# Performance work log

Hardware: AMD Instinct MI355X
Metric: run time of the kernel (lower is better)

The kernel has to match this reference:

```python
import jax, jax.numpy as jnp
import numpy as np

DELTA_V = 0.5
DELTA_D = 1.5
ALPHA = 1.0
BETA = 1.0
GAMMA = 0.001
K = 33  # segment count: id 0 = background, 1..32 = instances (matches fill_max)


def setup_inputs() -> dict:
    key = jax.random.key(0)
    k1, k2 = jax.random.split(key)
    embeddings = jax.random.normal(k1, (8, 16, 512, 512), dtype=jnp.float32)
    instance_masks = jax.random.randint(k2, (8, 512, 512), 0, K, dtype=jnp.int32)
    return {"embeddings": embeddings, "instance_masks": instance_masks}


def _safe_norm(sq):
    # sqrt with zero-safe gradient: returns 0 where sq == 0
    pos = sq > 0
    return jnp.sqrt(jnp.where(pos, sq, 1.0)) * pos.astype(sq.dtype)


def _per_image(emb, mask):
    # emb: (E, H, W), mask: (H, W)
    E = emb.shape[0]
    emb_flat = emb.reshape(E, -1).T            # (N, E)
    ids = mask.reshape(-1)                      # (N,)

    counts = jax.ops.segment_sum(jnp.ones(ids.shape, jnp.float32), ids, num_segments=K)  # (K,)
    sums = jax.ops.segment_sum(emb_flat, ids, num_segments=K)                             # (K, E)
    counts_c = jnp.maximum(counts, 1.0)
    means = sums / counts_c[:, None]            # (K, E)

    present = counts[1:] > 0                    # (K-1,) which instance ids appear
    n_inst = present.sum().astype(jnp.float32)

    # variance (pull) term: per-pixel distance to own instance mean
    diff = emb_flat - means[ids]                # (N, E)
    pix_d = _safe_norm(jnp.sum(diff * diff, axis=1))
    var_term = jnp.maximum(pix_d - DELTA_V, 0.0) ** 2
    var_per = jax.ops.segment_sum(var_term, ids, num_segments=K)[1:]  # drop background seg
    var_loss = jnp.sum(jnp.where(present, var_per / counts_c[1:], 0.0)) / jnp.maximum(n_inst, 1.0)

    # distance (push) term: pairwise centroid distances among present instances
    m = means[1:]                               # (K-1, E)
    dsq = jnp.sum((m[:, None, :] - m[None, :, :]) ** 2, axis=-1)
    dmat = _safe_norm(dsq)
    pair_mask = (jnp.triu(jnp.ones((K - 1, K - 1), bool), 1)
                 & present[:, None] & present[None, :])
    n_pairs = pair_mask.sum().astype(jnp.float32)
    dist_term = jnp.maximum(2.0 * DELTA_D - dmat, 0.0) ** 2
    dist_loss = jnp.sum(jnp.where(pair_mask, dist_term, 0.0)) / jnp.maximum(n_pairs, 1.0)
    dist_loss = dist_loss * (n_inst > 1.0).astype(jnp.float32)

    # regularization: mean centroid norm over present instances
    mean_norms = _safe_norm(jnp.sum(m * m, axis=1))
    reg_loss = jnp.sum(jnp.where(present, mean_norms, 0.0)) / jnp.maximum(n_inst, 1.0)

    valid = (n_inst > 0.0).astype(jnp.float32)
    return var_loss * valid, dist_loss * valid, reg_loss * valid, valid


def reference(embeddings, instance_masks):
    v, d, r, valid = jax.vmap(_per_image)(embeddings, instance_masks)
    vs = jnp.maximum(valid.sum(), 1.0)
    var_loss = v.sum() / vs
    dist_loss = d.sum() / vs
    reg_loss = r.sum() / vs
    total = ALPHA * var_loss + BETA * dist_loss + GAMMA * reg_loss
    return jnp.stack([total, var_loss, dist_loss, reg_loss])
```

## Files before the change

kernel.cpp:

```cpp
#include <hip/hip_runtime.h>
#include <math.h>


#define B 8
#define E 16
#define HW (512*512)
#define BLK 256
#define P1_BPI 128
#define P2_BPI 128
#define P2_VPB (HW / 4 / P2_BPI)

typedef __attribute__((ext_vector_type(8)))  short short8;
typedef __attribute__((ext_vector_type(16))) float floatx16;

__device__ __forceinline__ float atomAddF(float* p, float v) {
  return unsafeAtomicAdd(p, v);
}

__device__ __forceinline__ unsigned pack_bf(float a, float b) {
  return __builtin_amdgcn_perm(__float_as_uint(b), __float_as_uint(a), 0x07060302u);
}

__global__ __launch_bounds__(BLK) void pass1_kernel(
    const float* __restrict__ emb, const int* __restrict__ mask,
    float* __restrict__ gsum ) {
  __shared__ int4 mstage[4][128];
  __shared__ __align__(16) float lred[4][32][33];
  const int b    = blockIdx.y;
  const int t    = threadIdx.x;
  const int lane = t & 63;
  const int wv   = __builtin_amdgcn_readfirstlane(t >> 6);
  const int n    = lane & 31;
  const int h    = lane >> 5;
  const int myid = n + 1;
  const bool ld  = (n < 16);

  const int ppw    = HW / (P1_BPI * 4);
  const int ntiles = ppw / 16;
  const int base   = (blockIdx.x * 4 + wv) * ppw;

  {
    const int4* __restrict__ mg = (const int4*)(mask + (size_t)b * HW + base);
    mstage[wv][lane]      = mg[lane];
    mstage[wv][64 + lane] = mg[64 + lane];
  }
  __syncthreads();

  const float* __restrict__ pl = emb + ((size_t)b * E + (n & 15)) * HW + base + 8 * h;

  floatx16 acc;
#pragma unroll
  for (int i = 0; i < 16; ++i) acc[i] = 0.f;

  float4 fb[4][2];
#pragma unroll
  for (int u = 0; u < 4; ++u) {
    if (ld) {
      fb[u][0] = ((const float4*)(pl + u * 16))[0];
      fb[u][1] = ((const float4*)(pl + u * 16))[1];
    }
  }

  for (int tl4 = 0; tl4 < ntiles; tl4 += 4) {
#pragma unroll
    for (int u = 0; u < 4; ++u) {
      const int tl = tl4 + u;

      const int4 A0 = mstage[wv][tl * 4 + 2 * h];
      const int4 A1 = mstage[wv][tl * 4 + 2 * h + 1];

      short8 af;
      af[0] = (A0.x == myid) ? (short)0x3F80 : (short)0;
      af[1] = (A0.y == myid) ? (short)0x3F80 : (short)0;
      af[2] = (A0.z == myid) ? (short)0x3F80 : (short)0;
      af[3] = (A0.w == myid) ? (short)0x3F80 : (short)0;
      af[4] = (A1.x == myid) ? (short)0x3F80 : (short)0;
      af[5] = (A1.y == myid) ? (short)0x3F80 : (short)0;
      af[6] = (A1.z == myid) ? (short)0x3F80 : (short)0;
      af[7] = (A1.w == myid) ? (short)0x3F80 : (short)0;

      short8 bf;
      if (ld) {
        union { uint4 u4; short8 s; } cv;
        cv.u4.x = pack_bf(fb[u][0].x, fb[u][0].y);
        cv.u4.y = pack_bf(fb[u][0].z, fb[u][0].w);
        cv.u4.z = pack_bf(fb[u][1].x, fb[u][1].y);
        cv.u4.w = pack_bf(fb[u][1].z, fb[u][1].w);
        bf = cv.s;
      } else if (n == 16) {
        const short one = (short)0x3F80;
        bf[0]=one; bf[1]=one; bf[2]=one; bf[3]=one; bf[4]=one; bf[5]=one; bf[6]=one; bf[7]=one;
      } else {
        bf[0]=0; bf[1]=0; bf[2]=0; bf[3]=0; bf[4]=0; bf[5]=0; bf[6]=0; bf[7]=0;
      }

      acc = __builtin_amdgcn_mfma_f32_32x32x16_bf16(af, bf, acc, 0, 0, 0);

      const int tn = tl + 4;
      if (tn < ntiles && ld) {
        fb[u][0] = ((const float4*)(pl + tn * 16))[0];
        fb[u][1] = ((const float4*)(pl + tn * 16))[1];
      }
    }
  }

#pragma unroll
  for (int r = 0; r < 16; ++r) {
    const int row = (r & 3) + 8 * (r >> 2) + 4 * h;
    lred[wv][row][n] = acc[r];
  }
  __syncthreads();

  for (int i = t; i < 32 * 32; i += BLK) {
    const int row = i >> 5, col = i & 31;
    if (col < 17) {
      const float s = lred[0][row][col] + lred[1][row][col]
                    + lred[2][row][col] + lred[3][row][col];
      atomAddF(&gsum[((size_t)b * 32 + row) * 17 + col], s);
    }
  }
}

__global__ __launch_bounds__(BLK) void pass2_kernel(
    const float* __restrict__ emb, const int* __restrict__ mask,
    const float* __restrict__ gsum, float* __restrict__ vsum ) {
  __shared__ __align__(16) float mean4[33][4][4];
  __shared__ float winv[33];
  __shared__ float wred[4];
  const int b = blockIdx.y;
  const int t = threadIdx.x;

  for (int i = t; i < 33 * 16; i += BLK) {
    const int k = i >> 4, e = i & 15;
    float m = 0.f;
    if (k >= 1) {
      const float cnt = gsum[((size_t)b * 32 + (k - 1)) * 17 + 16];
      const float cc  = cnt > 1.f ? cnt : 1.f;
      m = gsum[((size_t)b * 32 + (k - 1)) * 17 + e] / cc;
    }
    const int j = e >> 2;
    mean4[k][(j + k + (k >> 2)) & 3][e & 3] = m;
  }
  if (t < 33) {
    float w = 0.f;
    if (t >= 1) {
      const float cnt = gsum[((size_t)b * 32 + (t - 1)) * 17 + 16];
      w = cnt > 0.5f ? 1.f / cnt : 0.f;
    }
    winv[t] = w;
  }
  __syncthreads();

  const int4*  __restrict__ maskv = (const int4*)(mask + (size_t)b * HW);
  const float* __restrict__ embb  = emb + (size_t)b * E * HW;
  const int v0 = blockIdx.x * P2_VPB;
  float vacc = 0.f;

#pragma unroll 1
  for (int v = v0 + t; v < v0 + P2_VPB; v += BLK) {
    const int4 id = maskv[v];
    float4 x[E];
#pragma unroll
    for (int e = 0; e < E; ++e) x[e] = ((const float4*)(embb + (size_t)e * HW))[v];

    const int sx = id.x + (id.x >> 2);
    const int sy = id.y + (id.y >> 2);
    const int sz = id.z + (id.z >> 2);
    const int sw = id.w + (id.w >> 2);

    float d0 = 0.f, d1 = 0.f, d2 = 0.f, d3 = 0.f;
#pragma unroll
    for (int j = 0; j < 4; ++j) {
      const float4 m0 = *(const float4*)&mean4[id.x][(j + sx) & 3][0];
      const float4 m1 = *(const float4*)&mean4[id.y][(j + sy) & 3][0];
      const float4 m2 = *(const float4*)&mean4[id.z][(j + sz) & 3][0];
      const float4 m3 = *(const float4*)&mean4[id.w][(j + sw) & 3][0];
      const float4 a0 = x[4 * j + 0], a1 = x[4 * j + 1];
      const float4 a2 = x[4 * j + 2], a3 = x[4 * j + 3];
      float u;
      u = a0.x - m0.x; d0 += u * u;  u = a1.x - m0.y; d0 += u * u;
      u = a2.x - m0.z; d0 += u * u;  u = a3.x - m0.w; d0 += u * u;
      u = a0.y - m1.x; d1 += u * u;  u = a1.y - m1.y; d1 += u * u;
      u = a2.y - m1.z; d1 += u * u;  u = a3.y - m1.w; d1 += u * u;
      u = a0.z - m2.x; d2 += u * u;  u = a1.z - m2.y; d2 += u * u;
      u = a2.z - m2.z; d2 += u * u;  u = a3.z - m2.w; d2 += u * u;
      u = a0.w - m3.x; d3 += u * u;  u = a1.w - m3.y; d3 += u * u;
      u = a2.w - m3.z; d3 += u * u;  u = a3.w - m3.w; d3 += u * u;
    }
    float hh;
    hh = fmaxf(sqrtf(d0) - 0.5f, 0.f); vacc += hh * hh * winv[id.x];
    hh = fmaxf(sqrtf(d1) - 0.5f, 0.f); vacc += hh * hh * winv[id.y];
    hh = fmaxf(sqrtf(d2) - 0.5f, 0.f); vacc += hh * hh * winv[id.z];
    hh = fmaxf(sqrtf(d3) - 0.5f, 0.f); vacc += hh * hh * winv[id.w];
  }

#pragma unroll
  for (int off = 32; off >= 1; off >>= 1) vacc += __shfl_down(vacc, off, 64);
  if ((t & 63) == 0) wred[t >> 6] = vacc;
  __syncthreads();
  if (t == 0) atomAddF(&vsum[b], wred[0] + wred[1] + wred[2] + wred[3]);
}

__global__ __launch_bounds__(BLK) void final_kernel(
    const float* __restrict__ gsum, const float* __restrict__ vsum,
    float* __restrict__ out) {
  __shared__ float mean[B][32][E];
  __shared__ float cnts[B][32];
  __shared__ float rb[B], db[B], pb[B], nb[B];
  const int t = threadIdx.x;

  if (t < B) { rb[t] = 0.f; db[t] = 0.f; pb[t] = 0.f; nb[t] = 0.f; }
  {
    const int bb = t >> 5, k = t & 31;
    const float c  = gsum[((size_t)bb * 32 + k) * 17 + 16];
    const float cc = c > 1.f ? c : 1.f;
    cnts[bb][k] = c;
#pragma unroll
    for (int e = 0; e < E; ++e)
      mean[bb][k][e] = gsum[((size_t)bb * 32 + k) * 17 + e] / cc;
  }
  __syncthreads();

  {
    const int bb = t >> 5, k = t & 31;
    const float c = cnts[bb][k];
    if (c > 0.5f) {
      atomAddF(&nb[bb], 1.f);
      float sq = 0.f;
#pragma unroll
      for (int e = 0; e < E; ++e) { const float m = mean[bb][k][e]; sq += m * m; }
      atomAddF(&rb[bb], sq > 0.f ? sqrtf(sq) : 0.f);
    }
  }
  __syncthreads();

  for (int idx = t; idx < B * 32 * 32; idx += BLK) {
    const int bb = idx >> 10;
    const int p  = idx & 1023;
    const int i  = p >> 5;
    const int j  = p & 31;
    if (i < j && cnts[bb][i] > 0.5f && cnts[bb][j] > 0.5f) {
      atomAddF(&pb[bb], 1.f);
      float sq = 0.f;
#pragma unroll
      for (int e = 0; e < E; ++e) {
        const float d = mean[bb][i][e] - mean[bb][j][e];
        sq += d * d;
      }
      const float dn = sq > 0.f ? sqrtf(sq) : 0.f;
      const float hh = 3.0f - dn;
      if (hh > 0.f) atomAddF(&db[bb], hh * hh);
    }
  }
  __syncthreads();

  if (t == 0) {
    float sv = 0.f, sd = 0.f, sr = 0.f, svalid = 0.f;
    for (int bb = 0; bb < B; ++bb) {
      const float ni  = nb[bb];
      const float nim = ni > 1.f ? ni : 1.f;
      const float var_b = vsum[bb] / nim;
      const float reg_b = rb[bb] / nim;
      const float npm   = pb[bb] > 1.f ? pb[bb] : 1.f;
      const float dist_b = (ni > 1.f) ? (db[bb] / npm) : 0.f;
      const float valid  = ni > 0.f ? 1.f : 0.f;
      sv += var_b * valid;
      sd += dist_b * valid;
      sr += reg_b * valid;
      svalid += valid;
    }
    const float vs = svalid > 1.f ? svalid : 1.f;
    const float var = sv / vs, dist = sd / vs, reg = sr / vs;
    out[0] = var + dist + 0.001f * reg;
    out[1] = var;
    out[2] = dist;
    out[3] = reg;
  }
}

extern "C" void kernel_launch(void* const* d_in, const int* in_sizes, int n_in,
                              void* d_out, int out_size, void* d_ws, size_t ws_size,
                              hipStream_t stream) {
  const float* emb  = (const float*)d_in[0];
  const int*   mask = (const int*)d_in[1];
  float* out = (float*)d_out;

  float* gsum = (float*)d_ws;
  float* vsum = (float*)((char*)d_ws + (size_t)B * 32 * 17 * 4);

  hipMemsetAsync(d_ws, 0, (size_t)(B * 32 * 17 + B) * 4, stream);

  pass1_kernel<<<dim3(P1_BPI, B), BLK, 0, stream>>>(emb, mask, gsum);
  pass2_kernel<<<dim3(P2_BPI, B), BLK, 0, stream>>>(emb, mask, gsum, vsum);
  final_kernel<<<1, BLK, 0, stream>>>(gsum, vsum, out);
}
```

Baseline: 249.6 us.

## Replace MFMA segment-sum with LDS atomic histogram and fuse final reduction via ticket

The bf16 MFMA-based per-instance summation is replaced by per-wave shared-memory float atomics into a 33x17 histogram, computed in fp32. The separate final kernel is folded into the hinge kernel with a global ticket counter, so the last block computes the pairwise distance, regularisation and output terms. Grid mapping is changed to each thread handling two float4 pixel groups. LDS atomics with 33 random ids may cause bank contention, and the last-block finalisation serialises some work at the tail.

```diff
diff --git a/kernel.cpp b/kernel.cpp
--- a/kernel.cpp
+++ b/kernel.cpp
@@ -5,130 +5,80 @@
 #define B 8
 #define E 16
 #define HW (512*512)
+#define HW4 (HW/4)
 #define BLK 256
-#define P1_BPI 128
-#define P2_BPI 128
-#define P2_VPB (HW / 4 / P2_BPI)
-
-typedef __attribute__((ext_vector_type(8)))  short short8;
-typedef __attribute__((ext_vector_type(16))) float floatx16;
+#define XBLK 128
+#define ITERS 2
+#define NBLOCKS (XBLK*B)
+
+#define VSUM_OFF   20480
+#define TICKET_OFF 24576
 
 __device__ __forceinline__ float atomAddF(float* p, float v) {
   return unsafeAtomicAdd(p, v);
 }
 
-__device__ __forceinline__ unsigned pack_bf(float a, float b) {
-  return __builtin_amdgcn_perm(__float_as_uint(b), __float_as_uint(a), 0x07060302u);
-}
-
-__global__ __launch_bounds__(BLK) void pass1_kernel(
+__global__ __launch_bounds__(BLK, 4) void hist_kernel(
     const float* __restrict__ emb, const int* __restrict__ mask,
     float* __restrict__ gsum ) {
-  __shared__ int4 mstage[4][128];
-  __shared__ __align__(16) float lred[4][32][33];
-  const int b    = blockIdx.y;
-  const int t    = threadIdx.x;
-  const int lane = t & 63;
-  const int wv   = __builtin_amdgcn_readfirstlane(t >> 6);
-  const int n    = lane & 31;
-  const int h    = lane >> 5;
-  const int myid = n + 1;
-  const bool ld  = (n < 16);
-
-  const int ppw    = HW / (P1_BPI * 4);
-  const int ntiles = ppw / 16;
-  const int base   = (blockIdx.x * 4 + wv) * ppw;
-
-  {
-    const int4* __restrict__ mg = (const int4*)(mask + (size_t)b * HW + base);
-    mstage[wv][lane]      = mg[lane];
-    mstage[wv][64 + lane] = mg[64 + lane];
-  }
-  __syncthreads();
-
-  const float* __restrict__ pl = emb + ((size_t)b * E + (n & 15)) * HW + base + 8 * h;
-
-  floatx16 acc;
-#pragma unroll
-  for (int i = 0; i < 16; ++i) acc[i] = 0.f;
-
-  float4 fb[4][2];
-#pragma unroll
-  for (int u = 0; u < 4; ++u) {
-    if (ld) {
-      fb[u][0] = ((const float4*)(pl + u * 16))[0];
-      fb[u][1] = ((const float4*)(pl + u * 16))[1];
-    }
-  }
-
-  for (int tl4 = 0; tl4 < ntiles; tl4 += 4) {
-#pragma unroll
-    for (int u = 0; u < 4; ++u) {
-      const int tl = tl4 + u;
-
-      const int4 A0 = mstage[wv][tl * 4 + 2 * h];
-      const int4 A1 = mstage[wv][tl * 4 + 2 * h + 1];
-
-      short8 af;
-      af[0] = (A0.x == myid) ? (short)0x3F80 : (short)0;
-      af[1] = (A0.y == myid) ? (short)0x3F80 : (short)0;
-      af[2] = (A0.z == myid) ? (short)0x3F80 : (short)0;
-      af[3] = (A0.w == myid) ? (short)0x3F80 : (short)0;
-      af[4] = (A1.x == myid) ? (short)0x3F80 : (short)0;
-      af[5] = (A1.y == myid) ? (short)0x3F80 : (short)0;
-      af[6] = (A1.z == myid) ? (short)0x3F80 : (short)0;
-      af[7] = (A1.w == myid) ? (short)0x3F80 : (short)0;
-
-      short8 bf;
-      if (ld) {
-        union { uint4 u4; short8 s; } cv;
-        cv.u4.x = pack_bf(fb[u][0].x, fb[u][0].y);
-        cv.u4.y = pack_bf(fb[u][0].z, fb[u][0].w);
-        cv.u4.z = pack_bf(fb[u][1].x, fb[u][1].y);
-        cv.u4.w = pack_bf(fb[u][1].z, fb[u][1].w);
-        bf = cv.s;
-      } else if (n == 16) {
-        const short one = (short)0x3F80;
-        bf[0]=one; bf[1]=one; bf[2]=one; bf[3]=one; bf[4]=one; bf[5]=one; bf[6]=one; bf[7]=one;
-      } else {
-        bf[0]=0; bf[1]=0; bf[2]=0; bf[3]=0; bf[4]=0; bf[5]=0; bf[6]=0; bf[7]=0;
-      }
-
-      acc = __builtin_amdgcn_mfma_f32_32x32x16_bf16(af, bf, acc, 0, 0, 0);
-
-      const int tn = tl + 4;
-      if (tn < ntiles && ld) {
-        fb[u][0] = ((const float4*)(pl + tn * 16))[0];
-        fb[u][1] = ((const float4*)(pl + tn * 16))[1];
-      }
-    }
-  }
-
-#pragma unroll
-  for (int r = 0; r < 16; ++r) {
-    const int row = (r & 3) + 8 * (r >> 2) + 4 * h;
-    lred[wv][row][n] = acc[r];
-  }
-  __syncthreads();
-
-  for (int i = t; i < 32 * 32; i += BLK) {
-    const int row = i >> 5, col = i & 31;
-    if (col < 17) {
-      const float s = lred[0][row][col] + lred[1][row][col]
-                    + lred[2][row][col] + lred[3][row][col];
-      atomAddF(&gsum[((size_t)b * 32 + row) * 17 + col], s);
-    }
-  }
-}
-
-__global__ __launch_bounds__(BLK) void pass2_kernel(
+  __shared__ float hist[4][33][17];
+  const int b  = blockIdx.y;
+  const int t  = threadIdx.x;
+  const int wv = t >> 6;
+
+  for (int i = t; i < 4 * 33 * 17; i += BLK) ((float*)hist)[i] = 0.f;
+  __syncthreads();
+
+  const int4*   __restrict__ maskv = (const int4*)(mask + (size_t)b * HW);
+  const float4* __restrict__ embv  = (const float4*)(emb + (size_t)b * E * HW);
+  const int gbase = blockIdx.x * (BLK * ITERS) + t;
+
+#pragma unroll
+  for (int it = 0; it < ITERS; ++it) {
+    const int g = gbase + it * BLK;
+    const int4 id = maskv[g];
+    float4 x[E];
+#pragma unroll
+    for (int e = 0; e < E; ++e) x[e] = embv[(size_t)e * HW4 + g];
+
+#pragma unroll
+    for (int e = 0; e < E; ++e) {
+      atomicAdd(&hist[wv][id.x][e], x[e].x);
+      atomicAdd(&hist[wv][id.y][e], x[e].y);
+      atomicAdd(&hist[wv][id.z][e], x[e].z);
+      atomicAdd(&hist[wv][id.w][e], x[e].w);
+    }
+    atomicAdd(&hist[wv][id.x][16], 1.f);
+    atomicAdd(&hist[wv][id.y][16], 1.f);
+    atomicAdd(&hist[wv][id.z][16], 1.f);
+    atomicAdd(&hist[wv][id.w][16], 1.f);
+  }
+  __syncthreads();
+
+  for (int i = t; i < 32 * 17; i += BLK) {
+    const int id = i / 17 + 1;
+    const int e  = i % 17;
+    const float s = hist[0][id][e] + hist[1][id][e]
+                  + hist[2][id][e] + hist[3][id][e];
+    atomAddF(&gsum[((size_t)b * 32 + (id - 1)) * 17 + e], s);
+  }
+}
+
+__global__ __launch_bounds__(BLK, 4) void hinge_kernel(
     const float* __restrict__ emb, const int* __restrict__ mask,
-    const float* __restrict__ gsum, float* __restrict__ vsum ) {
+    const float* __restrict__ gsum, float* __restrict__ vsum,
+    unsigned* __restrict__ ticket, float* __restrict__ out) {
   __shared__ __align__(16) float mean4[33][4][4];
   __shared__ float winv[33];
   __shared__ float wred[4];
+  __shared__ unsigned tkt;
+  __shared__ __align__(16) float c_mean[B][32][E];
+  __shared__ float c_cnt[B][32];
+  __shared__ float c_rb[B], c_db[B], c_pb[B], c_nb[B];
+
   const int b = blockIdx.y;
   const int t = threadIdx.x;
+  const int wv = t >> 6;
 
   for (int i = t; i < 33 * 16; i += BLK) {
     const int k = i >> 4, e = i & 15;
@@ -151,17 +101,18 @@
   }
   __syncthreads();
 
-  const int4*  __restrict__ maskv = (const int4*)(mask + (size_t)b * HW);
-  const float* __restrict__ embb  = emb + (size_t)b * E * HW;
-  const int v0 = blockIdx.x * P2_VPB;
+  const int4*   __restrict__ maskv = (const int4*)(mask + (size_t)b * HW);
+  const float4* __restrict__ embv  = (const float4*)(emb + (size_t)b * E * HW);
+  const int gbase = blockIdx.x * (BLK * ITERS) + t;
   float vacc = 0.f;
 
-#pragma unroll 1
-  for (int v = v0 + t; v < v0 + P2_VPB; v += BLK) {
-    const int4 id = maskv[v];
+#pragma unroll
+  for (int it = 0; it < ITERS; ++it) {
+    const int g = gbase + it * BLK;
+    const int4 id = maskv[g];
     float4 x[E];
 #pragma unroll
-    for (int e = 0; e < E; ++e) x[e] = ((const float4*)(embb + (size_t)e * HW))[v];
+    for (int e = 0; e < E; ++e) x[e] = embv[(size_t)e * HW4 + g];
 
     const int sx = id.x + (id.x >> 2);
     const int sy = id.y + (id.y >> 2);
@@ -196,60 +147,71 @@
 
 #pragma unroll
   for (int off = 32; off >= 1; off >>= 1) vacc += __shfl_down(vacc, off, 64);
-  if ((t & 63) == 0) wred[t >> 6] = vacc;
-  __syncthreads();
-  if (t == 0) atomAddF(&vsum[b], wred[0] + wred[1] + wred[2] + wred[3]);
-}
-
-__global__ __launch_bounds__(BLK) void final_kernel(
-    const float* __restrict__ gsum, const float* __restrict__ vsum,
-    float* __restrict__ out) {
-  __shared__ float mean[B][32][E];
-  __shared__ float cnts[B][32];
-  __shared__ float rb[B], db[B], pb[B], nb[B];
-  const int t = threadIdx.x;
-
-  if (t < B) { rb[t] = 0.f; db[t] = 0.f; pb[t] = 0.f; nb[t] = 0.f; }
+  if ((t & 63) == 0) wred[wv] = vacc;
+  __syncthreads();
+
+  if (t == 0) {
+    atomAddF(&vsum[b], wred[0] + wred[1] + wred[2] + wred[3]);
+    __threadfence();
+    tkt = atomicAdd(ticket, 1u);
+  }
+  __syncthreads();
+  if (tkt != NBLOCKS - 1) return;
+
+  __threadfence();
   {
     const int bb = t >> 5, k = t & 31;
     const float c  = gsum[((size_t)bb * 32 + k) * 17 + 16];
     const float cc = c > 1.f ? c : 1.f;
-    cnts[bb][k] = c;
+    c_cnt[bb][k] = c;
 #pragma unroll
     for (int e = 0; e < E; ++e)
-      mean[bb][k][e] = gsum[((size_t)bb * 32 + k) * 17 + e] / cc;
-  }
+      c_mean[bb][k][e] = gsum[((size_t)bb * 32 + k) * 17 + e] / cc;
+  }
+  if (t < B) { c_rb[t] = 0.f; c_db[t] = 0.f; c_pb[t] = 0.f; c_nb[t] = 0.f; }
   __syncthreads();
 
   {
     const int bb = t >> 5, k = t & 31;
-    const float c = cnts[bb][k];
+    const float c = c_cnt[bb][k];
     if (c > 0.5f) {
-      atomAddF(&nb[bb], 1.f);
+      atomicAdd(&c_nb[bb], 1.f);
       float sq = 0.f;
 #pragma unroll
-      for (int e = 0; e < E; ++e) { const float m = mean[bb][k][e]; sq += m * m; }
-      atomAddF(&rb[bb], sq > 0.f ? sqrtf(sq) : 0.f);
-    }
-  }
-  __syncthreads();
-
-  for (int idx = t; idx < B * 32 * 32; idx += BLK) {
-    const int bb = idx >> 10;
-    const int p  = idx & 1023;
-    const int i  = p >> 5;
-    const int j  = p & 31;
-    if (i < j && cnts[bb][i] > 0.5f && cnts[bb][j] > 0.5f) {
-      atomAddF(&pb[bb], 1.f);
-      float sq = 0.f;
-#pragma unroll
-      for (int e = 0; e < E; ++e) {
-        const float d = mean[bb][i][e] - mean[bb][j][e];
-        sq += d * d;
+      for (int e = 0; e < E; ++e) { const float m = c_mean[bb][k][e]; sq += m * m; }
+      atomicAdd(&c_rb[bb], sq > 0.f ? sqrtf(sq) : 0.f);
+    }
+  }
+
+  for (int bb = 0; bb < B; ++bb) {
+    float dacc = 0.f, pacc = 0.f;
+    for (int p = t; p < 32 * 32; p += BLK) {
+      const int i = p >> 5, j = p & 31;
+      if (i < j && c_cnt[bb][i] > 0.5f && c_cnt[bb][j] > 0.5f) {
+        pacc += 1.f;
+        const float4* mi = (const float4*)&c_mean[bb][i][0];
+        const float4* mj = (const float4*)&c_mean[bb][j][0];
+        float sq = 0.f;
+#pragma unroll
+        for (int q = 0; q < 4; ++q) {
+          const float4 a = mi[q], c4 = mj[q];
+          float u;
+          u = a.x - c4.x; sq += u * u;  u = a.y - c4.y; sq += u * u;
+          u = a.z - c4.z; sq += u * u;  u = a.w - c4.w; sq += u * u;
+        }
+        const float dn = sq > 0.f ? sqrtf(sq) : 0.f;
+        const float hh = 3.0f - dn;
+        if (hh > 0.f) dacc += hh * hh;
       }
-      const float dn = sq > 0.f ? sqrtf(sq) : 0.f;
-      const float hh = 3.0f - dn;
-      if (hh > 0.f) atomAddF(&db[bb], hh * hh);
+    }
+#pragma unroll
+    for (int off = 32; off >= 1; off >>= 1) {
+      dacc += __shfl_down(dacc, off, 64);
+      pacc += __shfl_down(pacc, off, 64);
+    }
+    if ((t & 63) == 0) {
+      atomicAdd(&c_db[bb], dacc);
+      atomicAdd(&c_pb[bb], pacc);
     }
   }
   __syncthreads();
@@ -257,12 +219,14 @@
   if (t == 0) {
     float sv = 0.f, sd = 0.f, sr = 0.f, svalid = 0.f;
     for (int bb = 0; bb < B; ++bb) {
-      const float ni  = nb[bb];
+      const float vb = __hip_atomic_load(&vsum[bb], __ATOMIC_RELAXED,
+                                         __HIP_MEMORY_SCOPE_AGENT);
+      const float ni  = c_nb[bb];
       const float nim = ni > 1.f ? ni : 1.f;
-      const float var_b = vsum[bb] / nim;
-      const float reg_b = rb[bb] / nim;
-      const float npm   = pb[bb] > 1.f ? pb[bb] : 1.f;
-      const float dist_b = (ni > 1.f) ? (db[bb] / npm) : 0.f;
+      const float var_b = vb / nim;
+      const float reg_b = c_rb[bb] / nim;
+      const float npm   = c_pb[bb] > 1.f ? c_pb[bb] : 1.f;
+      const float dist_b = (ni > 1.f) ? (c_db[bb] / npm) : 0.f;
       const float valid  = ni > 0.f ? 1.f : 0.f;
       sv += var_b * valid;
       sd += dist_b * valid;
@@ -285,12 +249,12 @@
   const int*   mask = (const int*)d_in[1];
   float* out = (float*)d_out;
 
-  float* gsum = (float*)d_ws;
-  float* vsum = (float*)((char*)d_ws + (size_t)B * 32 * 17 * 4);
-
-  hipMemsetAsync(d_ws, 0, (size_t)(B * 32 * 17 + B) * 4, stream);
-
-  pass1_kernel<<<dim3(P1_BPI, B), BLK, 0, stream>>>(emb, mask, gsum);
-  pass2_kernel<<<dim3(P2_BPI, B), BLK, 0, stream>>>(emb, mask, gsum, vsum);
-  final_kernel<<<1, BLK, 0, stream>>>(gsum, vsum, out);
-}
+  float*    gsum   = (float*)d_ws;
+  float*    vsum   = (float*)((char*)d_ws + VSUM_OFF);
+  unsigned* ticket = (unsigned*)((char*)d_ws + TICKET_OFF);
+
+  hipMemsetAsync(d_ws, 0, 28672, stream);
+
+  hist_kernel <<<dim3(XBLK, B), BLK, 0, stream>>>(emb, mask, gsum);
+  hinge_kernel<<<dim3(XBLK, B), BLK, 0, stream>>>(emb, mask, gsum, vsum, ticket, out);
+}
```

Result: slower. 400.9 us (+60.6%).

## Cache bf16 pixel-major embeddings in pass1 and fuse final reduction into pass2

Applied to the files above, without the earlier changes.

Pass1 now writes a bf16, pixel-major transposed copy of the embeddings to workspace as a side effect of its MFMA packing. Pass2 reads this half-size copy instead of the fp32 input, which cuts the second pass's HBM traffic roughly in half but adds a write in pass1. The separate final kernel is removed: the last block, found with an atomic ticket, does the centroid pair and regularisation math, which saves a launch. Computing the variance term from bf16 values lowers precision.

```diff
diff --git a/kernel.cpp b/kernel.cpp
--- a/kernel.cpp
+++ b/kernel.cpp
@@ -5,10 +5,16 @@
 #define B 8
 #define E 16
 #define HW (512*512)
+#define HW4 (HW/4)
 #define BLK 256
 #define P1_BPI 128
-#define P2_BPI 128
-#define P2_VPB (HW / 4 / P2_BPI)
+#define P2_XBLK 512
+#define NBLOCKS (P2_XBLK * B)
+
+#define VSUM_OFF   20480
+#define TICKET_OFF 24576
+#define EMB16_OFF  32768
+#define WS_ZERO    25088
 
 typedef __attribute__((ext_vector_type(8)))  short short8;
 typedef __attribute__((ext_vector_type(16))) float floatx16;
@@ -16,16 +22,21 @@
 __device__ __forceinline__ float atomAddF(float* p, float v) {
   return unsafeAtomicAdd(p, v);
 }
-
 __device__ __forceinline__ unsigned pack_bf(float a, float b) {
   return __builtin_amdgcn_perm(__float_as_uint(b), __float_as_uint(a), 0x07060302u);
 }
+__device__ __forceinline__ float blo(unsigned u) { return __uint_as_float(u << 16); }
+__device__ __forceinline__ float bhi(unsigned u) { return __uint_as_float(u & 0xFFFF0000u); }
+__device__ __forceinline__ float gldA(const float* p) {
+  return __hip_atomic_load(p, __ATOMIC_RELAXED, __HIP_MEMORY_SCOPE_AGENT);
+}
 
 __global__ __launch_bounds__(BLK) void pass1_kernel(
     const float* __restrict__ emb, const int* __restrict__ mask,
-    float* __restrict__ gsum ) {
+    float* __restrict__ gsum , unsigned* __restrict__ emb16) {
   __shared__ int4 mstage[4][128];
   __shared__ __align__(16) float lred[4][32][33];
+  __shared__ unsigned tpose[4][128];
   const int b    = blockIdx.y;
   const int t    = threadIdx.x;
   const int lane = t & 63;
@@ -87,6 +98,10 @@
         cv.u4.z = pack_bf(fb[u][1].x, fb[u][1].y);
         cv.u4.w = pack_bf(fb[u][1].z, fb[u][1].w);
         bf = cv.s;
+        tpose[wv][(4 * h + 0) * 16 + n] = cv.u4.x;
+        tpose[wv][(4 * h + 1) * 16 + n] = cv.u4.y;
+        tpose[wv][(4 * h + 2) * 16 + n] = cv.u4.z;
+        tpose[wv][(4 * h + 3) * 16 + n] = cv.u4.w;
       } else if (n == 16) {
         const short one = (short)0x3F80;
         bf[0]=one; bf[1]=one; bf[2]=one; bf[3]=one; bf[4]=one; bf[5]=one; bf[6]=one; bf[7]=one;
@@ -101,6 +116,13 @@
         fb[u][0] = ((const float4*)(pl + tn * 16))[0];
         fb[u][1] = ((const float4*)(pl + tn * 16))[1];
       }
+
+      {
+        uint2 w;
+        w.x = tpose[wv][2 * lane];
+        w.y = tpose[wv][2 * lane + 1];
+        ((uint2*)emb16)[((size_t)b * HW + base + tl * 16) * 4 + lane] = w;
+      }
     }
   }
 
@@ -122,13 +144,20 @@
 }
 
 __global__ __launch_bounds__(BLK) void pass2_kernel(
-    const float* __restrict__ emb, const int* __restrict__ mask,
-    const float* __restrict__ gsum, float* __restrict__ vsum ) {
+    const unsigned* __restrict__ emb16, const int* __restrict__ mask,
+    const float* __restrict__ gsum, float* __restrict__ vsum,
+    unsigned* __restrict__ ticket, float* __restrict__ out) {
   __shared__ __align__(16) float mean4[33][4][4];
   __shared__ float winv[33];
   __shared__ float wred[4];
-  const int b = blockIdx.y;
-  const int t = threadIdx.x;
+  __shared__ unsigned tkt;
+  __shared__ __align__(16) float c_mean[B][32][E];
+  __shared__ float c_cnt[B][32];
+  __shared__ float c_rb[B], c_db[B], c_pb[B], c_nb[B];
+
+  const int b  = blockIdx.y;
+  const int t  = threadIdx.x;
+  const int wv = t >> 6;
 
   for (int i = t; i < 33 * 16; i += BLK) {
     const int k = i >> 4, e = i & 15;
@@ -151,105 +180,107 @@
   }
   __syncthreads();
 
-  const int4*  __restrict__ maskv = (const int4*)(mask + (size_t)b * HW);
-  const float* __restrict__ embb  = emb + (size_t)b * E * HW;
-  const int v0 = blockIdx.x * P2_VPB;
-  float vacc = 0.f;
-
-#pragma unroll 1
-  for (int v = v0 + t; v < v0 + P2_VPB; v += BLK) {
-    const int4 id = maskv[v];
-    float4 x[E];
-#pragma unroll
-    for (int e = 0; e < E; ++e) x[e] = ((const float4*)(embb + (size_t)e * HW))[v];
-
-    const int sx = id.x + (id.x >> 2);
-    const int sy = id.y + (id.y >> 2);
-    const int sz = id.z + (id.z >> 2);
-    const int sw = id.w + (id.w >> 2);
-
-    float d0 = 0.f, d1 = 0.f, d2 = 0.f, d3 = 0.f;
-#pragma unroll
-    for (int j = 0; j < 4; ++j) {
-      const float4 m0 = *(const float4*)&mean4[id.x][(j + sx) & 3][0];
-      const float4 m1 = *(const float4*)&mean4[id.y][(j + sy) & 3][0];
-      const float4 m2 = *(const float4*)&mean4[id.z][(j + sz) & 3][0];
-      const float4 m3 = *(const float4*)&mean4[id.w][(j + sw) & 3][0];
-      const float4 a0 = x[4 * j + 0], a1 = x[4 * j + 1];
-      const float4 a2 = x[4 * j + 2], a3 = x[4 * j + 3];
-      float u;
-      u = a0.x - m0.x; d0 += u * u;  u = a1.x - m0.y; d0 += u * u;
-      u = a2.x - m0.z; d0 += u * u;  u = a3.x - m0.w; d0 += u * u;
-      u = a0.y - m1.x; d1 += u * u;  u = a1.y - m1.y; d1 += u * u;
-      u = a2.y - m1.z; d1 += u * u;  u = a3.y - m1.w; d1 += u * u;
-      u = a0.z - m2.x; d2 += u * u;  u = a1.z - m2.y; d2 += u * u;
-      u = a2.z - m2.z; d2 += u * u;  u = a3.z - m2.w; d2 += u * u;
-      u = a0.w - m3.x; d3 += u * u;  u = a1.w - m3.y; d3 += u * u;
-      u = a2.w - m3.z; d3 += u * u;  u = a3.w - m3.w; d3 += u * u;
-    }
-    float hh;
-    hh = fmaxf(sqrtf(d0) - 0.5f, 0.f); vacc += hh * hh * winv[id.x];
-    hh = fmaxf(sqrtf(d1) - 0.5f, 0.f); vacc += hh * hh * winv[id.y];
-    hh = fmaxf(sqrtf(d2) - 0.5f, 0.f); vacc += hh * hh * winv[id.z];
-    hh = fmaxf(sqrtf(d3) - 0.5f, 0.f); vacc += hh * hh * winv[id.w];
-  }
+  const int pp = blockIdx.x * BLK + t;
+  const int2 id2 = ((const int2*)(mask + (size_t)b * HW))[pp];
+  const uint4* __restrict__ cp = (const uint4*)emb16 + ((size_t)b * (HW / 2) + pp) * 4;
+  const uint4 U0 = cp[0], U1 = cp[1], U2 = cp[2], U3 = cp[3];
+
+  const int ide = id2.x, ido = id2.y;
+  const int se = ide + (ide >> 2);
+  const int so = ido + (ido >> 2);
+  float de = 0.f, dd = 0.f;
+
+#define JBLK(UU, jj) do {                                                 \
+    const float4 me = *(const float4*)&mean4[ide][((jj) + se) & 3][0];    \
+    const float4 mo = *(const float4*)&mean4[ido][((jj) + so) & 3][0];    \
+    float u_;                                                             \
+    u_ = blo(UU.x) - me.x; de += u_ * u_;                                 \
+    u_ = bhi(UU.x) - mo.x; dd += u_ * u_;                                 \
+    u_ = blo(UU.y) - me.y; de += u_ * u_;                                 \
+    u_ = bhi(UU.y) - mo.y; dd += u_ * u_;                                 \
+    u_ = blo(UU.z) - me.z; de += u_ * u_;                                 \
+    u_ = bhi(UU.z) - mo.z; dd += u_ * u_;                                 \
+    u_ = blo(UU.w) - me.w; de += u_ * u_;                                 \
+    u_ = bhi(UU.w) - mo.w; dd += u_ * u_;                                 \
+  } while (0)
+
+  JBLK(U0, 0);
+  JBLK(U1, 1);
+  JBLK(U2, 2);
+  JBLK(U3, 3);
+#undef JBLK
+
+  float vacc = 0.f, hh;
+  hh = fmaxf(sqrtf(de) - 0.5f, 0.f); vacc += hh * hh * winv[ide];
+  hh = fmaxf(sqrtf(dd) - 0.5f, 0.f); vacc += hh * hh * winv[ido];
 
 #pragma unroll
   for (int off = 32; off >= 1; off >>= 1) vacc += __shfl_down(vacc, off, 64);
-  if ((t & 63) == 0) wred[t >> 6] = vacc;
-  __syncthreads();
-  if (t == 0) atomAddF(&vsum[b], wred[0] + wred[1] + wred[2] + wred[3]);
-}
-
-__global__ __launch_bounds__(BLK) void final_kernel(
-    const float* __restrict__ gsum, const float* __restrict__ vsum,
-    float* __restrict__ out) {
-  __shared__ float mean[B][32][E];
-  __shared__ float cnts[B][32];
-  __shared__ float rb[B], db[B], pb[B], nb[B];
-  const int t = threadIdx.x;
-
-  if (t < B) { rb[t] = 0.f; db[t] = 0.f; pb[t] = 0.f; nb[t] = 0.f; }
+  if ((t & 63) == 0) wred[wv] = vacc;
+  __syncthreads();
+
+  if (t == 0) {
+    atomAddF(&vsum[b], wred[0] + wred[1] + wred[2] + wred[3]);
+    __threadfence();
+    tkt = atomicAdd(ticket, 1u);
+  }
+  __syncthreads();
+  if (tkt != NBLOCKS - 1) return;
+
+  __threadfence();
   {
     const int bb = t >> 5, k = t & 31;
-    const float c  = gsum[((size_t)bb * 32 + k) * 17 + 16];
+    const float c  = gldA(&gsum[((size_t)bb * 32 + k) * 17 + 16]);
     const float cc = c > 1.f ? c : 1.f;
-    cnts[bb][k] = c;
+    c_cnt[bb][k] = c;
 #pragma unroll
     for (int e = 0; e < E; ++e)
-      mean[bb][k][e] = gsum[((size_t)bb * 32 + k) * 17 + e] / cc;
-  }
+      c_mean[bb][k][e] = gldA(&gsum[((size_t)bb * 32 + k) * 17 + e]) / cc;
+  }
+  if (t < B) { c_rb[t] = 0.f; c_db[t] = 0.f; c_pb[t] = 0.f; c_nb[t] = 0.f; }
   __syncthreads();
 
   {
     const int bb = t >> 5, k = t & 31;
-    const float c = cnts[bb][k];
+    const float c = c_cnt[bb][k];
     if (c > 0.5f) {
-      atomAddF(&nb[bb], 1.f);
+      atomicAdd(&c_nb[bb], 1.f);
       float sq = 0.f;
 #pragma unroll
-      for (int e = 0; e < E; ++e) { const float m = mean[bb][k][e]; sq += m * m; }
-      atomAddF(&rb[bb], sq > 0.f ? sqrtf(sq) : 0.f);
-    }
-  }
-  __syncthreads();
-
-  for (int idx = t; idx < B * 32 * 32; idx += BLK) {
-    const int bb = idx >> 10;
-    const int p  = idx & 1023;
-    const int i  = p >> 5;
-    const int j  = p & 31;
-    if (i < j && cnts[bb][i] > 0.5f && cnts[bb][j] > 0.5f) {
-      atomAddF(&pb[bb], 1.f);
-      float sq = 0.f;
-#pragma unroll
-      for (int e = 0; e < E; ++e) {
-        const float d = mean[bb][i][e] - mean[bb][j][e];
-        sq += d * d;
+      for (int e = 0; e < E; ++e) { const float m = c_mean[bb][k][e]; sq += m * m; }
+      atomicAdd(&c_rb[bb], sq > 0.f ? sqrtf(sq) : 0.f);
+    }
+  }
+
+  for (int bb = 0; bb < B; ++bb) {
+    float dacc = 0.f, pacc = 0.f;
+    for (int p = t; p < 32 * 32; p += BLK) {
+      const int i = p >> 5, j = p & 31;
+      if (i < j && c_cnt[bb][i] > 0.5f && c_cnt[bb][j] > 0.5f) {
+        pacc += 1.f;
+        const float4* mi = (const float4*)&c_mean[bb][i][0];
+        const float4* mj = (const float4*)&c_mean[bb][j][0];
+        float sq = 0.f;
+#pragma unroll
+        for (int q = 0; q < 4; ++q) {
+          const float4 a = mi[q], c4 = mj[q];
+          float u;
+          u = a.x - c4.x; sq += u * u;  u = a.y - c4.y; sq += u * u;
+          u = a.z - c4.z; sq += u * u;  u = a.w - c4.w; sq += u * u;
+        }
+        const float dn = sq > 0.f ? sqrtf(sq) : 0.f;
+        const float hh2 = 3.0f - dn;
+        if (hh2 > 0.f) dacc += hh2 * hh2;
       }
-      const float dn = sq > 0.f ? sqrtf(sq) : 0.f;
-      const float hh = 3.0f - dn;
-      if (hh > 0.f) atomAddF(&db[bb], hh * hh);
+    }
+#pragma unroll
+    for (int off = 32; off >= 1; off >>= 1) {
+      dacc += __shfl_down(dacc, off, 64);
+      pacc += __shfl_down(pacc, off, 64);
+    }
+    if ((t & 63) == 0) {
+      atomicAdd(&c_db[bb], dacc);
+      atomicAdd(&c_pb[bb], pacc);
     }
   }
   __syncthreads();
@@ -257,12 +288,13 @@
   if (t == 0) {
     float sv = 0.f, sd = 0.f, sr = 0.f, svalid = 0.f;
     for (int bb = 0; bb < B; ++bb) {
-      const float ni  = nb[bb];
+      const float vbv = gldA(&vsum[bb]);
+      const float ni  = c_nb[bb];
       const float nim = ni > 1.f ? ni : 1.f;
-      const float var_b = vsum[bb] / nim;
-      const float reg_b = rb[bb] / nim;
-      const float npm   = pb[bb] > 1.f ? pb[bb] : 1.f;
-      const float dist_b = (ni > 1.f) ? (db[bb] / npm) : 0.f;
+      const float var_b = vbv / nim;
+      const float reg_b = c_rb[bb] / nim;
+      const float npm   = c_pb[bb] > 1.f ? c_pb[bb] : 1.f;
+      const float dist_b = (ni > 1.f) ? (c_db[bb] / npm) : 0.f;
       const float valid  = ni > 0.f ? 1.f : 0.f;
       sv += var_b * valid;
       sd += dist_b * valid;
@@ -285,12 +317,13 @@
   const int*   mask = (const int*)d_in[1];
   float* out = (float*)d_out;
 
-  float* gsum = (float*)d_ws;
-  float* vsum = (float*)((char*)d_ws + (size_t)B * 32 * 17 * 4);
-
-  hipMemsetAsync(d_ws, 0, (size_t)(B * 32 * 17 + B) * 4, stream);
-
-  pass1_kernel<<<dim3(P1_BPI, B), BLK, 0, stream>>>(emb, mask, gsum);
-  pass2_kernel<<<dim3(P2_BPI, B), BLK, 0, stream>>>(emb, mask, gsum, vsum);
-  final_kernel<<<1, BLK, 0, stream>>>(gsum, vsum, out);
-}
+  float*    gsum  = (float*)d_ws;
+  float*    vsum  = (float*)((char*)d_ws + VSUM_OFF);
+  unsigned* ticket= (unsigned*)((char*)d_ws + TICKET_OFF);
+  unsigned* emb16 = (unsigned*)((char*)d_ws + EMB16_OFF);
+
+  hipMemsetAsync(d_ws, 0, WS_ZERO, stream);
+
+  pass1_kernel<<<dim3(P1_BPI, B), BLK, 0, stream>>>(emb, mask, gsum, emb16);
+  pass2_kernel<<<dim3(P2_XBLK, B), BLK, 0, stream>>>(emb16, mask, gsum, vsum, ticket, out);
+}
```

Result: slower. 348.9 us (+39.7%).
